# Performance work log

Hardware: AMD Instinct MI355X
Metric: run time of the kernel (lower is better)

The kernel has to match this reference:

```python
import math
import jax, jax.numpy as jnp
import numpy as np

B, N, D, H, R = 2, 2048, 1024, 16, 32
DK = D // H  # 64


def _alibi_slopes(n_heads):
    def pow2slopes(n):
        start = 2 ** (-(2 ** (-(math.log2(n) - 3))))
        return [start * (start ** i) for i in range(n)]
    if math.log2(n_heads).is_integer():
        vals = pow2slopes(n_heads)
    else:
        closest = 2 ** math.floor(math.log2(n_heads))
        vals = pow2slopes(closest)
        vals += pow2slopes(2 * closest)[0::2][: n_heads - closest]
    return np.asarray(vals, dtype=np.float32)


def _alibi_bias(n_heads, n_tokens):
    # bias[h, i, j] = -slope[h] * max(j - i, 0)
    i = np.arange(n_tokens)[:, None]
    j = np.arange(n_tokens)[None, :]
    dist = np.clip(j - i, 0, None).astype(np.float32)
    return jnp.asarray(-_alibi_slopes(n_heads)[:, None, None] * dist)  # [H, N, N]


def setup_inputs() -> dict:
    key = jax.random.key(0)
    ks = jax.random.split(key, 6)
    s = 0.02
    return {
        "x": jax.random.normal(ks[0], (B, N, D), dtype=jnp.float32),
        "mask": jnp.zeros((1, 1, N, N), dtype=jnp.float32),
        "W_q": jax.random.normal(ks[1], (D, D), dtype=jnp.float32) * s,
        "W_k": jax.random.normal(ks[2], (D, D), dtype=jnp.float32) * s,
        "W_v": jax.random.normal(ks[3], (D, D), dtype=jnp.float32) * s,
        "U": jax.random.normal(ks[4], (DK, R), dtype=jnp.float32) * (1.0 / math.sqrt(DK)),
        "W_proj": jax.random.normal(ks[5], (D, D), dtype=jnp.float32) * s,
        "rel_bias_tokens": N,
    }


def reference(x, mask, W_q, W_k, W_v, U, W_proj, rel_bias_tokens):
    b, n, d = x.shape
    dk = U.shape[0]
    h = d // dk
    # q/k: Linear (no bias) -> split heads -> low-rank projection via U: [b,h,n,r]
    q = jnp.einsum("bnhd,dr->bhnr", (x @ W_q.T).reshape(b, n, h, dk), U)
    k = jnp.einsum("bnhd,dr->bhnr", (x @ W_k.T).reshape(b, n, h, dk), U)
    v = (x @ W_v.T).reshape(b, n, h, dk).transpose(0, 2, 1, 3)  # [b,h,n,dk]
    # note: scale uses sqrt(dk), not sqrt(r) (custom scale from the module)
    att = jnp.einsum("bhnr,bhmr->bhnm", q, k) / math.sqrt(dk)
    bias = _alibi_bias(h, rel_bias_tokens)  # [h, N_total, N_total]
    att = att + bias[None, :, -n:, :] + mask
    p = jax.nn.softmax(att, axis=-1)
    z = jnp.einsum("bhnm,bhmd->bnhd", p, v).reshape(b, n, h * dk)
    return z @ W_proj.T  # dropout is identity at inference
```

## Files before the change

### kernel.cpp

```cpp
#include <hip/hip_runtime.h>
#include <cstdint>

#define DEV __device__ __forceinline__

typedef __bf16 bf16x8 __attribute__((ext_vector_type(8)));
typedef float f32x4 __attribute__((ext_vector_type(4)));
typedef unsigned short u16x4 __attribute__((ext_vector_type(4)));
typedef unsigned short u16x8 __attribute__((ext_vector_type(8)));
typedef float f32x4v __attribute__((ext_vector_type(4)));

DEV unsigned short f2bf(float f) {
  union { float f; unsigned int u; } v; v.f = f;
  unsigned int r = v.u + 0x7fffu + ((v.u >> 16) & 1u);
  return (unsigned short)(r >> 16);
}

DEV void gl2lds16(const void* g, void* l) {
  __builtin_amdgcn_global_load_lds(
      (const __attribute__((address_space(1))) void*)g,
      (__attribute__((address_space(3))) void*)l, 16, 0, 0);
}

DEV bf16x8 ld8(const unsigned short* p) { return *(const bf16x8*)p; }


__global__ __launch_bounds__(256) void prep(
    const float* __restrict__ x, const float* __restrict__ Wp,
    const float* __restrict__ Wv, const float* __restrict__ Wq,
    const float* __restrict__ Wk, const float* __restrict__ U,
    unsigned short* __restrict__ xb, unsigned short* __restrict__ Wpb,
    unsigned short* __restrict__ Wcat) {
  __shared__ float Us[64 * 32];
  const int bx = blockIdx.x, t = threadIdx.x;
  if (bx < 6144) {
    const float* s; unsigned short* d; int i;
    if (bx < 4096)      { s = x;  d = xb;               i = bx * 256 + t; }
    else if (bx < 5120) { s = Wp; d = Wpb;              i = (bx - 4096) * 256 + t; }
    else                { s = Wv; d = Wcat + 1024*1024; i = (bx - 5120) * 256 + t; }
    f32x4v f = ((const f32x4v*)s)[i];
    u16x4 u;
    u[0] = f2bf(f[0]); u[1] = f2bf(f[1]); u[2] = f2bf(f[2]); u[3] = f2bf(f[3]);
    ((u16x4*)d)[i] = u;
  } else {
    ((f32x4v*)Us)[t] = ((const f32x4v*)U)[t];
    ((f32x4v*)Us)[t + 256] = ((const f32x4v*)U)[t + 256];
    __syncthreads();
    int gid = (bx - 6144) * 256 + t;
    int d = gid & 1023;
    int tmp = gid >> 10;
    int rq = tmp & 7, hh = (tmp >> 3) & 15, qk = tmp >> 7;
    const float* W = qk ? Wk : Wq;
    const float* wp = W + (size_t)(hh * 64) * 1024 + d;
    f32x4v acc = {0.f, 0.f, 0.f, 0.f};
    #pragma unroll 8
    for (int dk = 0; dk < 64; dk++) {
      float wv = wp[(size_t)dk * 1024];
      acc += (*(const f32x4v*)(Us + dk * 32 + rq * 4)) * wv;
    }
    float sc = qk ? 1.0f : 0.18033688011112042f;
    int orow = qk * 512 + hh * 32 + rq * 4;
    #pragma unroll
    for (int i = 0; i < 4; i++)
      Wcat[(size_t)(orow + i) * 1024 + d] = f2bf(acc[i] * sc);
  }
}


template <int OUTF32>
__global__ __launch_bounds__(256) void gemm_bt(
    const unsigned short* __restrict__ A, const unsigned short* __restrict__ Bt,
    void* __restrict__ Cout, int M, int Nc, int K) {
  __shared__ __align__(16) unsigned short As[2][128 * 32];
  __shared__ __align__(16) unsigned short Bs[2][128 * 32];
  const int t = threadIdx.x;
  const int w = t >> 6, lane = t & 63;
  const int quad = lane >> 4, l15 = lane & 15;
  const int row0 = blockIdx.y * 128, col0 = blockIdx.x * 128;
  const int wr = (w >> 1) * 64, wc = (w & 1) * 64;

  f32x4 acc[4][4];
  #pragma unroll
  for (int i = 0; i < 4; i++)
    #pragma unroll
    for (int j = 0; j < 4; j++) acc[i][j] = (f32x4){0.f, 0.f, 0.f, 0.f};

  const int srow = t >> 2;
  const int swz = ((t & 3) ^ (srow & 3)) * 8;
  const unsigned short* ga0 = A + (size_t)(row0 + srow) * K + swz;
  const unsigned short* ga1 = ga0 + (size_t)64 * K;
  const unsigned short* gb0 = Bt + (size_t)(col0 + srow) * K + swz;
  const unsigned short* gb1 = gb0 + (size_t)64 * K;
  const int lofs0 = (w * 16) * 32, lofs1 = (64 + w * 16) * 32;

  gl2lds16(ga0, &As[0][lofs0]);
  gl2lds16(ga1, &As[0][lofs1]);
  gl2lds16(gb0, &Bs[0][lofs0]);
  gl2lds16(gb1, &Bs[0][lofs1]);

  int cur = 0;
  for (int k0 = 0; k0 < K; k0 += 32, cur ^= 1) {
    __syncthreads();
    if (k0 + 32 < K) {
      gl2lds16(ga0 + k0 + 32, &As[cur ^ 1][lofs0]);
      gl2lds16(ga1 + k0 + 32, &As[cur ^ 1][lofs1]);
      gl2lds16(gb0 + k0 + 32, &Bs[cur ^ 1][lofs0]);
      gl2lds16(gb1 + k0 + 32, &Bs[cur ^ 1][lofs1]);
    }
    bf16x8 af[4], bfr[4];
    #pragma unroll
    for (int i = 0; i < 4; i++)
      af[i] = ld8(&As[cur][(wr + i * 16 + l15) * 32 + ((quad ^ (l15 & 3)) << 3)]);
    #pragma unroll
    for (int j = 0; j < 4; j++)
      bfr[j] = ld8(&Bs[cur][(wc + j * 16 + l15) * 32 + ((quad ^ (l15 & 3)) << 3)]);
    #pragma unroll
    for (int i = 0; i < 4; i++)
      #pragma unroll
      for (int j = 0; j < 4; j++)
        acc[i][j] = __builtin_amdgcn_mfma_f32_16x16x32_bf16(af[i], bfr[j], acc[i][j], 0, 0, 0);
  }

  #pragma unroll
  for (int i = 0; i < 4; i++)
    #pragma unroll
    for (int j = 0; j < 4; j++) {
      int r = row0 + wr + i * 16 + quad * 4;
      int c = col0 + wc + j * 16 + l15;
      #pragma unroll
      for (int reg = 0; reg < 4; reg++) {
        if (OUTF32) ((float*)Cout)[(size_t)(r + reg) * Nc + c] = acc[i][j][reg];
        else ((unsigned short*)Cout)[(size_t)(r + reg) * Nc + c] = f2bf(acc[i][j][reg]);
      }
    }
}


__global__ __launch_bounds__(256) void vt_transpose(
    const unsigned short* __restrict__ QKV, unsigned short* __restrict__ Vt) {
  __shared__ unsigned short Lt[64][72];
  const int bh = blockIdx.y, tok0 = blockIdx.x * 64;
  const int b = bh >> 4, h = bh & 15;
  const int t = threadIdx.x;
  const int row = t & 63, dkg = t >> 6;
  const unsigned short* src = QKV + (size_t)(b * 2048 + tok0 + row) * 2048 + 1024 + h * 64 + dkg * 16;
  u16x8 v0 = *(const u16x8*)src;
  u16x8 v1 = *(const u16x8*)(src + 8);
  #pragma unroll
  for (int i = 0; i < 8; i++) {
    Lt[dkg * 16 + i][row] = v0[i];
    Lt[dkg * 16 + 8 + i][row] = v1[i];
  }
  __syncthreads();
  const int dk = t >> 2, part = t & 3;
  unsigned short* dst = Vt + (size_t)(bh * 64 + dk) * 2048;
  #pragma unroll
  for (int s2 = 0; s2 < 2; s2++) {
    int n = tok0 + part * 16 + s2 * 8;
    int c = (n >> 3) & 15;
    int phys = (n & ~127) | ((c ^ (dk & 15)) << 3);
    u16x8 vv;
    #pragma unroll
    for (int i = 0; i < 8; i++) vv[i] = Lt[dk][part * 16 + s2 * 8 + i];
    *(u16x8*)(dst + phys) = vv;
  }
}


__global__ __launch_bounds__(512, 4) void flash_attn(
    const unsigned short* __restrict__ QKV, const unsigned short* __restrict__ Vtg,
    unsigned short* __restrict__ Z) {
  __shared__ __align__(16) unsigned short Ps[128 * 128];
  __shared__ __align__(16) unsigned short Ks[2][128 * 32];
  __shared__ __align__(16) unsigned short Vs[2][64 * 128];

  const int f = blockIdx.x;
  const int xx = f & 7, jj0 = f >> 3;
  const int a = jj0 >> 4, jq = jj0 & 15;
  const int g = xx + 8 * a;
  const int b = g & 1, h = g >> 1;
  const int qt = (a < 2) ? jq : (15 - jq);

  const int t = threadIdx.x;
  const int w = t >> 6, lane = t & 63;
  const int quad = lane >> 4, l15 = lane & 15;
  const int srow = t >> 2;
  const int swz = ((t & 3) ^ (srow & 3)) * 8;
  const int xr = l15 & 7, qh = quad >> 1, qlo = quad & 1;

  const float slope2 = exp2f(-0.5f * (float)(h + 1)) * 1.4426950408889634f;
  const float slope16 = slope2 * 16.0f;
  int ktend = qt + (int)((15.0f / slope2 + 127.0f) * 0.0078125f);
  if (ktend > 15) ktend = 15;

  const unsigned short* Qg = QKV + (size_t)(b * 2048 + qt * 128) * 2048 + h * 32;
  const unsigned short* Kg = QKV + (size_t)(b * 2048) * 2048 + 512 + h * 32;
  const unsigned short* Vg = Vtg + (size_t)((b * 16 + h) * 64) * 2048;

  gl2lds16(Qg + (size_t)srow * 2048 + swz, &Ks[1][(w * 16) * 32]);
  gl2lds16(Kg + (size_t)srow * 2048 + swz, &Ks[0][(w * 16) * 32]);
  gl2lds16(Vg + (size_t)(t >> 4) * 2048 + (t & 15) * 8, &Vs[0][(w * 4) * 128]);
  gl2lds16(Vg + (size_t)(32 + (t >> 4)) * 2048 + (t & 15) * 8, &Vs[0][(32 + w * 4) * 128]);
  __syncthreads();
  bf16x8 qf = ld8(&Ks[1][(w * 16 + l15) * 32 + ((quad ^ (l15 & 3)) << 3)]);

  f32x4 o[4];
  #pragma unroll
  for (int j = 0; j < 4; j++) o[j] = (f32x4){0.f, 0.f, 0.f, 0.f};
  f32x4 lacc = (f32x4){0.f, 0.f, 0.f, 0.f};
  bf16x8 onesf;
  #pragma unroll
  for (int i = 0; i < 8; i++) onesf[i] = (__bf16)1.0f;

  f32x4 base0;
  #pragma unroll
  for (int r = 0; r < 4; r++) base0[r] = slope2 * (float)(w * 16 + l15 - quad * 4 - r);
  const int dbase0 = quad * 4 - w * 16 - l15;

  unsigned short* pst = Ps + (w * 16 + l15) * 128 + qlo * 4;
  const f32x4 zero4 = (f32x4){0.f, 0.f, 0.f, 0.f};

  for (int kt = 0; kt <= ktend; kt++) {
    __syncthreads();
    const unsigned short* ksc = Ks[kt & 1];
    const unsigned short* vsc = Vs[kt & 1];
    if (kt < ktend) {
      unsigned short* ksn = Ks[(kt + 1) & 1];
      unsigned short* vsn = Vs[(kt + 1) & 1];
      gl2lds16(Kg + (size_t)((kt + 1) * 128 + srow) * 2048 + swz, &ksn[(w * 16) * 32]);
      gl2lds16(Vg + (size_t)(t >> 4) * 2048 + (kt + 1) * 128 + (t & 15) * 8, &vsn[(w * 4) * 128]);
      gl2lds16(Vg + (size_t)(32 + (t >> 4)) * 2048 + (kt + 1) * 128 + (t & 15) * 8,
               &vsn[(32 + w * 4) * 128]);
    }

    f32x4 s[8];
    if (kt > qt) {
      float off = slope2 * 128.0f * (float)(kt - qt);
      #pragma unroll
      for (int ct = 0; ct < 8; ct++) {
        bf16x8 kf = ld8(&ksc[(ct * 16 + l15) * 32 + ((quad ^ (l15 & 3)) << 3)]);
        float cc = off + slope16 * (float)ct;
        f32x4 ci;
        ci[0] = base0[0] - cc; ci[1] = base0[1] - cc;
        ci[2] = base0[2] - cc; ci[3] = base0[3] - cc;
        s[ct] = __builtin_amdgcn_mfma_f32_16x16x32_bf16(kf, qf, ci, 0, 0, 0);
      }
    } else {
      #pragma unroll
      for (int ct = 0; ct < 8; ct++) {
        bf16x8 kf = ld8(&ksc[(ct * 16 + l15) * 32 + ((quad ^ (l15 & 3)) << 3)]);
        s[ct] = __builtin_amdgcn_mfma_f32_16x16x32_bf16(kf, qf, zero4, 0, 0, 0);
      }
      if (kt == qt) {
        #pragma unroll
        for (int ct = 0; ct < 8; ct++)
          #pragma unroll
          for (int r = 0; r < 4; r++) {
            float d = (float)(ct * 16 + dbase0 + r);
            s[ct][r] += fminf(-slope2 * d, 0.0f);
          }
      }
    }

    #pragma unroll
    for (int ct = 0; ct < 8; ct++) {
      u16x4 pk;
      #pragma unroll
      for (int r = 0; r < 4; r++) {
        union { float f; unsigned u; } pu;
        pu.f = __builtin_amdgcn_exp2f(s[ct][r]);
        pk[r] = (unsigned short)(pu.u >> 16);
      }
      *(u16x4*)(pst + (((ct * 2 + qh) ^ xr) << 3)) = pk;
    }

    #pragma unroll
    for (int ks = 0; ks < 4; ks++) {
      bf16x8 pf = ld8(&Ps[(w * 16 + l15) * 128 + (((ks * 4 + quad) ^ xr) << 3)]);
      lacc = __builtin_amdgcn_mfma_f32_16x16x32_bf16(onesf, pf, lacc, 0, 0, 0);
      #pragma unroll
      for (int j = 0; j < 4; j++) {
        bf16x8 vf = ld8(&vsc[(j * 16 + l15) * 128 + (((ks * 4 + quad) ^ l15) << 3)]);
        o[j] = __builtin_amdgcn_mfma_f32_16x16x32_bf16(vf, pf, o[j], 0, 0, 0);
      }
    }
  }

  float linv = 1.0f / lacc[0];
  size_t zrow = ((size_t)(b * 2048 + qt * 128 + w * 16 + l15)) * 1024 + h * 64;
  #pragma unroll
  for (int j = 0; j < 4; j++) {
    u16x4 v4;
    #pragma unroll
    for (int reg = 0; reg < 4; reg++) v4[reg] = f2bf(o[j][reg] * linv);
    *(u16x4*)(Z + zrow + j * 16 + quad * 4) = v4;
  }
}


extern "C" void kernel_launch(void* const* d_in, const int* in_sizes, int n_in,
                              void* d_out, int out_size, void* d_ws, size_t ws_size,
                              hipStream_t stream) {
  const float* x  = (const float*)d_in[0];
  const float* Wq = (const float*)d_in[2];
  const float* Wk = (const float*)d_in[3];
  const float* Wv = (const float*)d_in[4];
  const float* U  = (const float*)d_in[5];
  const float* Wp = (const float*)d_in[6];
  float* out = (float*)d_out;

  char* ws = (char*)d_ws;
  unsigned short* xb   = (unsigned short*)(ws);
  unsigned short* Vtg  = (unsigned short*)(ws);
  unsigned short* Wcat = (unsigned short*)(ws + 8u * 1024 * 1024);
  unsigned short* Wpb  = (unsigned short*)(ws + 12u * 1024 * 1024);
  unsigned short* QKV  = (unsigned short*)(ws + 14u * 1024 * 1024);
  unsigned short* Zb   = (unsigned short*)(ws + 30u * 1024 * 1024);

  prep<<<7168, 256, 0, stream>>>(x, Wp, Wv, Wq, Wk, U, xb, Wpb, Wcat);
  gemm_bt<0><<<dim3(16, 32), 256, 0, stream>>>(xb, Wcat, QKV, 4096, 2048, 1024);
  vt_transpose<<<dim3(32, 32), 256, 0, stream>>>(QKV, Vtg);
  flash_attn<<<512, 512, 0, stream>>>(QKV, Vtg, Zb);
  gemm_bt<1><<<dim3(8, 32), 256, 0, stream>>>(Zb, Wpb, out, 4096, 1024, 1024);
}
```

Measured before the change: 202.0 us.

## Fuse V transpose into QKV GEMM epilogue, rebalance attention schedule, add setprio

The QKV GEMM now writes the V half of its output straight into the swizzled transposed V layout, so the separate transpose kernel and its extra pass over V are removed. QKV is stored with a 1024-wide row that holds only Q and K. Flash-attention blocks are remapped to (head, query-tile) through a per-XCD lookup meant to balance the uneven work that comes from the per-head ALiBi cutoff. MFMA sections are wrapped in s_setprio raises. In exchange, the epilogue writes for V become scattered 8-byte stores, and the block mapping is more complex.

```diff
diff --git a/kernel.cpp b/kernel.cpp
--- a/kernel.cpp
+++ b/kernel.cpp
@@ -66,10 +66,11 @@
 }
 
 
-template <int OUTF32>
+template <int OUTF32, int VW>
 __global__ __launch_bounds__(256) void gemm_bt(
     const unsigned short* __restrict__ A, const unsigned short* __restrict__ Bt,
-    void* __restrict__ Cout, int M, int Nc, int K) {
+    void* __restrict__ Cout, unsigned short* __restrict__ Vt,
+    int M, int Nc, int K) {
   __shared__ __align__(16) unsigned short As[2][128 * 32];
   __shared__ __align__(16) unsigned short Bs[2][128 * 32];
   const int t = threadIdx.x;
@@ -120,48 +121,37 @@
         acc[i][j] = __builtin_amdgcn_mfma_f32_16x16x32_bf16(af[i], bfr[j], acc[i][j], 0, 0, 0);
   }
 
-  #pragma unroll
-  for (int i = 0; i < 4; i++)
-    #pragma unroll
-    for (int j = 0; j < 4; j++) {
+  if (VW && blockIdx.x >= 8) {
+    #pragma unroll
+    for (int i = 0; i < 4; i++) {
       int r = row0 + wr + i * 16 + quad * 4;
-      int c = col0 + wc + j * 16 + l15;
-      #pragma unroll
-      for (int reg = 0; reg < 4; reg++) {
-        if (OUTF32) ((float*)Cout)[(size_t)(r + reg) * Nc + c] = acc[i][j][reg];
-        else ((unsigned short*)Cout)[(size_t)(r + reg) * Nc + c] = f2bf(acc[i][j][reg]);
-      }
-    }
-}
-
-
-__global__ __launch_bounds__(256) void vt_transpose(
-    const unsigned short* __restrict__ QKV, unsigned short* __restrict__ Vt) {
-  __shared__ unsigned short Lt[64][72];
-  const int bh = blockIdx.y, tok0 = blockIdx.x * 64;
-  const int b = bh >> 4, h = bh & 15;
-  const int t = threadIdx.x;
-  const int row = t & 63, dkg = t >> 6;
-  const unsigned short* src = QKV + (size_t)(b * 2048 + tok0 + row) * 2048 + 1024 + h * 64 + dkg * 16;
-  u16x8 v0 = *(const u16x8*)src;
-  u16x8 v1 = *(const u16x8*)(src + 8);
-  #pragma unroll
-  for (int i = 0; i < 8; i++) {
-    Lt[dkg * 16 + i][row] = v0[i];
-    Lt[dkg * 16 + 8 + i][row] = v1[i];
-  }
-  __syncthreads();
-  const int dk = t >> 2, part = t & 3;
-  unsigned short* dst = Vt + (size_t)(bh * 64 + dk) * 2048;
-  #pragma unroll
-  for (int s2 = 0; s2 < 2; s2++) {
-    int n = tok0 + part * 16 + s2 * 8;
-    int c = (n >> 3) & 15;
-    int phys = (n & ~127) | ((c ^ (dk & 15)) << 3);
-    u16x8 vv;
-    #pragma unroll
-    for (int i = 0; i < 8; i++) vv[i] = Lt[dk][part * 16 + s2 * 8 + i];
-    *(u16x8*)(dst + phys) = vv;
+      int bb = r >> 11, n = r & 2047;
+      int chunk = (n >> 3) & 15;
+      int nbase = (n & ~127) | (n & 4);
+      #pragma unroll
+      for (int j = 0; j < 4; j++) {
+        int vcol = col0 + wc + j * 16 + l15 - 1024;
+        int hh = vcol >> 6, dk = vcol & 63;
+        int phys = nbase | ((chunk ^ (dk & 15)) << 3);
+        u16x4 pk;
+        #pragma unroll
+        for (int reg = 0; reg < 4; reg++) pk[reg] = f2bf(acc[i][j][reg]);
+        *(u16x4*)(Vt + (size_t)((bb * 16 + hh) * 64 + dk) * 2048 + phys) = pk;
+      }
+    }
+  } else {
+    #pragma unroll
+    for (int i = 0; i < 4; i++)
+      #pragma unroll
+      for (int j = 0; j < 4; j++) {
+        int r = row0 + wr + i * 16 + quad * 4;
+        int c = col0 + wc + j * 16 + l15;
+        #pragma unroll
+        for (int reg = 0; reg < 4; reg++) {
+          if (OUTF32) ((float*)Cout)[(size_t)(r + reg) * Nc + c] = acc[i][j][reg];
+          else ((unsigned short*)Cout)[(size_t)(r + reg) * Nc + c] = f2bf(acc[i][j][reg]);
+        }
+      }
   }
 }
 
@@ -174,11 +164,28 @@
   __shared__ __align__(16) unsigned short Vs[2][64 * 128];
 
   const int f = blockIdx.x;
-  const int xx = f & 7, jj0 = f >> 3;
-  const int a = jj0 >> 4, jq = jj0 & 15;
-  const int g = xx + 8 * a;
-  const int b = g & 1, h = g >> 1;
-  const int qt = (a < 2) ? jq : (15 - jq);
+  const int xcd = f & 7, slot = f >> 3;
+  int rk = (slot < 32) ? slot : 95 - slot;
+  const int set = xcd >> 1;
+  const int b = xcd & 1;
+  const unsigned hpack = (set == 0) ? 0x0D0A0400u : (set == 1) ? 0x0C0B0601u
+                        : (set == 2) ? 0x0F090502u : 0x0E080703u;
+  const unsigned dpack = (set == 0) ? 0x0B040101u : (set == 1) ? 0x08060101u
+                        : (set == 2) ? 0x15030101u : 0x0F020201u;
+  int h = 0, qt = 0, done = 0;
+  #pragma unroll
+  for (int c = 16; c >= 2; --c) {
+    #pragma unroll
+    for (int a = 0; a < 4; ++a) {
+      int dh = (int)((dpack >> (8 * a)) & 0xFFu);
+      int cnt, qv;
+      if (c == 16) { cnt = (dh + 1 > 16) ? 16 : dh + 1; qv = 15 - rk; }
+      else         { qv = c - 1 - dh; cnt = (qv >= 0) ? 1 : 0; }
+      int take = (done == 0) && (rk < cnt);
+      if (take) { h = (int)((hpack >> (8 * a)) & 0xFFu); qt = qv; done = 1; }
+      if (!done) rk -= cnt;
+    }
+  }
 
   const int t = threadIdx.x;
   const int w = t >> 6, lane = t & 63;
@@ -192,12 +199,12 @@
   int ktend = qt + (int)((15.0f / slope2 + 127.0f) * 0.0078125f);
   if (ktend > 15) ktend = 15;
 
-  const unsigned short* Qg = QKV + (size_t)(b * 2048 + qt * 128) * 2048 + h * 32;
-  const unsigned short* Kg = QKV + (size_t)(b * 2048) * 2048 + 512 + h * 32;
+  const unsigned short* Qg = QKV + (size_t)(b * 2048 + qt * 128) * 1024 + h * 32;
+  const unsigned short* Kg = QKV + (size_t)(b * 2048) * 1024 + 512 + h * 32;
   const unsigned short* Vg = Vtg + (size_t)((b * 16 + h) * 64) * 2048;
 
-  gl2lds16(Qg + (size_t)srow * 2048 + swz, &Ks[1][(w * 16) * 32]);
-  gl2lds16(Kg + (size_t)srow * 2048 + swz, &Ks[0][(w * 16) * 32]);
+  gl2lds16(Qg + (size_t)srow * 1024 + swz, &Ks[1][(w * 16) * 32]);
+  gl2lds16(Kg + (size_t)srow * 1024 + swz, &Ks[0][(w * 16) * 32]);
   gl2lds16(Vg + (size_t)(t >> 4) * 2048 + (t & 15) * 8, &Vs[0][(w * 4) * 128]);
   gl2lds16(Vg + (size_t)(32 + (t >> 4)) * 2048 + (t & 15) * 8, &Vs[0][(32 + w * 4) * 128]);
   __syncthreads();
@@ -226,7 +233,7 @@
     if (kt < ktend) {
       unsigned short* ksn = Ks[(kt + 1) & 1];
       unsigned short* vsn = Vs[(kt + 1) & 1];
-      gl2lds16(Kg + (size_t)((kt + 1) * 128 + srow) * 2048 + swz, &ksn[(w * 16) * 32]);
+      gl2lds16(Kg + (size_t)((kt + 1) * 128 + srow) * 1024 + swz, &ksn[(w * 16) * 32]);
       gl2lds16(Vg + (size_t)(t >> 4) * 2048 + (kt + 1) * 128 + (t & 15) * 8, &vsn[(w * 4) * 128]);
       gl2lds16(Vg + (size_t)(32 + (t >> 4)) * 2048 + (kt + 1) * 128 + (t & 15) * 8,
                &vsn[(32 + w * 4) * 128]);
@@ -235,6 +242,7 @@
     f32x4 s[8];
     if (kt > qt) {
       float off = slope2 * 128.0f * (float)(kt - qt);
+      __builtin_amdgcn_s_setprio(1);
       #pragma unroll
       for (int ct = 0; ct < 8; ct++) {
         bf16x8 kf = ld8(&ksc[(ct * 16 + l15) * 32 + ((quad ^ (l15 & 3)) << 3)]);
@@ -244,12 +252,15 @@
         ci[2] = base0[2] - cc; ci[3] = base0[3] - cc;
         s[ct] = __builtin_amdgcn_mfma_f32_16x16x32_bf16(kf, qf, ci, 0, 0, 0);
       }
+      __builtin_amdgcn_s_setprio(0);
     } else {
+      __builtin_amdgcn_s_setprio(1);
       #pragma unroll
       for (int ct = 0; ct < 8; ct++) {
         bf16x8 kf = ld8(&ksc[(ct * 16 + l15) * 32 + ((quad ^ (l15 & 3)) << 3)]);
         s[ct] = __builtin_amdgcn_mfma_f32_16x16x32_bf16(kf, qf, zero4, 0, 0, 0);
       }
+      __builtin_amdgcn_s_setprio(0);
       if (kt == qt) {
         #pragma unroll
         for (int ct = 0; ct < 8; ct++)
@@ -273,6 +284,7 @@
       *(u16x4*)(pst + (((ct * 2 + qh) ^ xr) << 3)) = pk;
     }
 
+    __builtin_amdgcn_s_setprio(1);
     #pragma unroll
     for (int ks = 0; ks < 4; ks++) {
       bf16x8 pf = ld8(&Ps[(w * 16 + l15) * 128 + (((ks * 4 + quad) ^ xr) << 3)]);
@@ -283,6 +295,7 @@
         o[j] = __builtin_amdgcn_mfma_f32_16x16x32_bf16(vf, pf, o[j], 0, 0, 0);
       }
     }
+    __builtin_amdgcn_s_setprio(0);
   }
 
   float linv = 1.0f / lacc[0];
@@ -310,15 +323,14 @@
 
   char* ws = (char*)d_ws;
   unsigned short* xb   = (unsigned short*)(ws);
-  unsigned short* Vtg  = (unsigned short*)(ws);
   unsigned short* Wcat = (unsigned short*)(ws + 8u * 1024 * 1024);
   unsigned short* Wpb  = (unsigned short*)(ws + 12u * 1024 * 1024);
   unsigned short* QKV  = (unsigned short*)(ws + 14u * 1024 * 1024);
-  unsigned short* Zb   = (unsigned short*)(ws + 30u * 1024 * 1024);
+  unsigned short* Zb   = (unsigned short*)(ws + 22u * 1024 * 1024);
+  unsigned short* Vtg  = (unsigned short*)(ws + 30u * 1024 * 1024);
 
   prep<<<7168, 256, 0, stream>>>(x, Wp, Wv, Wq, Wk, U, xb, Wpb, Wcat);
-  gemm_bt<0><<<dim3(16, 32), 256, 0, stream>>>(xb, Wcat, QKV, 4096, 2048, 1024);
-  vt_transpose<<<dim3(32, 32), 256, 0, stream>>>(QKV, Vtg);
+  gemm_bt<0, 1><<<dim3(16, 32), 256, 0, stream>>>(xb, Wcat, QKV, Vtg, 4096, 1024, 1024);
   flash_attn<<<512, 512, 0, stream>>>(QKV, Vtg, Zb);
-  gemm_bt<1><<<dim3(8, 32), 256, 0, stream>>>(Zb, Wpb, out, 4096, 1024, 1024);
-}
+  gemm_bt<1, 0><<<dim3(8, 32), 256, 0, stream>>>(Zb, Wpb, out, nullptr, 4096, 1024, 1024);
+}
```

After: 190.8 us. 1.06x faster.
